# Optimization experiments

Hardware: AMD Instinct MI355X
Metric: run time of the kernel (lower is better)

## Reference

```python
import jax, jax.numpy as jnp
import numpy as np

N, n, D1, D2 = 16, 1024, 64, 64


def setup_inputs() -> dict:
    key = jax.random.key(0)
    ks = jax.random.split(key, 17)
    f = lambda k, shape: jax.random.normal(k, shape, dtype=jnp.float32)
    return {
        "A": f(ks[0], (N, n, n)),
        "X": f(ks[1], (N, n, D1)),
        "coeffs": f(ks[2], (5,)),
        "wA1": f(ks[3], (1, D1)),
        "wA2": f(ks[4], (1, D1)),
        "w11": f(ks[5], (D2, D1)),
        "w12": f(ks[6], (D2, D1)),
        "w13": f(ks[7], (D2, 1)),
        "w14": f(ks[8], (D2, 1)),
        "w15": f(ks[9], (D2, 1)),
        "w16": f(ks[10], (D2, 1)),
        "w21": f(ks[11], (D2, D1)),
        "w22": f(ks[12], (D2, D1)),
        "w23": f(ks[13], (D2, 1)),
        "w24": f(ks[14], (D2, 1)),
        "w25": f(ks[15], (D2, 1)),
        "w26": f(ks[16], (D2, 1)),
    }


def reference(A, X, coeffs, wA1, wA2, w11, w12, w13, w14, w15, w16,
              w21, w22, w23, w24, w25, w26):
    nn_ = A.shape[-1]
    diag = jnp.diagonal(A, axis1=-2, axis2=-1)          # (N, n)
    mean_diag = diag.mean(-1)                            # (N,)
    rowmean = A.mean(-1)                                 # (N, n) mean over columns
    mean_all = rowmean.mean(-1)                          # (N,)
    mean_X = X.mean(1)                                   # (N, D1)

    p1 = X @ wA1[0]                                      # (N, n)   Linear(D1->1) per node
    p2 = mean_X @ wA2[0]                                 # (N,)     Linear(D1->1) on mean

    # adjacency transform: scalar-weighted A + scalar stats + symmetrized row stats
    A_t = (coeffs[0] * A
           + (coeffs[1] * mean_all + coeffs[2] * mean_diag + p2)[:, None, None]
           + coeffs[3] * (rowmean[:, None, :] + rowmean[:, :, None])
           + coeffs[4] * (diag[:, None, :] + diag[:, :, None])
           + p1[:, None, :] + p1[:, :, None])             # (N, n, n)

    def node_transform(w_x, w_mx, w_col, w_diag, w_mdiag, w_mall):
        per_graph = (mean_X @ w_mx.T                      # (N, D2)
                     + mean_diag[:, None] * w_mdiag[:, 0][None, :]
                     + mean_all[:, None] * w_mall[:, 0][None, :])
        return (jnp.einsum('bnd,ed->bne', X, w_x)         # (N, n, D2)
                + rowmean[:, :, None] * w_col[:, 0]
                + diag[:, :, None] * w_diag[:, 0]
                + per_graph[:, None, :])

    X1_t = node_transform(w11, w12, w13, w14, w15, w16)
    X2_t = node_transform(w21, w22, w23, w24, w25, w26)

    out = A_t @ X2_t / nn_ + X1_t                         # (N, n, D2)
    return (A_t, out)
```

## Files before the change

### kernel.cpp

```cpp
#include <hip/hip_runtime.h>
#include <hip/hip_bf16.h>

#define NGRAPH 16
#define NNODE 1024
#define DDIM 64

typedef __attribute__((ext_vector_type(8))) short bf16x8;
typedef __attribute__((ext_vector_type(4))) float f32x4;

#define OFF_ROWSUM 0
#define OFF_DIAG   16384
#define OFF_P1     32768
#define OFF_R      49152
#define OFF_CS     65536
#define OFF_S      73728
#define OFF_S2P    75840
#define OFF_R2P    92224
#define OFF_BASE0  110656
#define OFF_X2T    1159232

__device__ __forceinline__ unsigned short f2bf(float f) {
    unsigned int u = __float_as_uint(f);
    u = (u + 0x7fffu + ((u >> 16) & 1u)) >> 16;
    return (unsigned short)u;
}

__device__ __forceinline__ float wave_reduce(float v) {
    #pragma unroll
    for (int off = 32; off; off >>= 1) v += __shfl_down(v, off, 64);
    return v;
}

__global__ __launch_bounds__(256) void kA_stats(const float* __restrict__ A,
                                                const float* __restrict__ X,
                                                const float* __restrict__ wA1,
                                                float* __restrict__ rowsum,
                                                float* __restrict__ diagv,
                                                float* __restrict__ p1,
                                                float* __restrict__ colsum_part) {
    if (blockIdx.x < NGRAPH * NNODE / 4) {
        int row  = blockIdx.x * 4 + (threadIdx.x >> 6);
        int lane = threadIdx.x & 63;
        const float4* b4 = (const float4*)(A + (size_t)row * NNODE);
        float sum = 0.f;
        #pragma unroll
        for (int it = 0; it < 4; ++it) {
            float4 v = b4[lane + it * 64];
            sum += v.x + v.y + v.z + v.w;
        }
        sum = wave_reduce(sum);
        if (lane == 0) {
            rowsum[row] = sum;
            int i = row & (NNODE - 1);
            diagv[row] = ((const float*)b4)[i];
        }
    } else {
        int bid  = blockIdx.x - NGRAPH * NNODE / 4;
        int b    = bid >> 3;
        int blk  = bid & 7;
        int wv   = threadIdx.x >> 6;
        int lane = threadIdx.x & 63;
        float w = wA1[lane];
        float cs = 0.f;
        int row0 = blk * 128 + wv * 32;
        const float* Xb = X + (size_t)b * NNODE * DDIM;
        for (int rI = 0; rI < 32; ++rI) {
            int i = row0 + rI;
            float x = Xb[i * DDIM + lane];
            cs += x;
            float v = wave_reduce(x * w);
            if (lane == 0) p1[b * NNODE + i] = v;
        }
        __shared__ float csl[4][64];
        csl[wv][lane] = cs;
        __syncthreads();
        if (threadIdx.x < 64) {
            float t = csl[0][lane] + csl[1][lane] + csl[2][lane] + csl[3][lane];
            colsum_part[(b * 8 + blk) * 64 + lane] = t;
        }
    }
}

__global__ __launch_bounds__(256) void kB_nodes(const float* __restrict__ X,
                                                const float* __restrict__ coeffs,
                                                const float* __restrict__ wA2,
                                                const float* __restrict__ w11,
                                                const float* __restrict__ w12,
                                                const float* __restrict__ w13,
                                                const float* __restrict__ w14,
                                                const float* __restrict__ w15,
                                                const float* __restrict__ w16,
                                                const float* __restrict__ w21,
                                                const float* __restrict__ w22,
                                                const float* __restrict__ w23,
                                                const float* __restrict__ w24,
                                                const float* __restrict__ w25,
                                                const float* __restrict__ w26,
                                                const float* __restrict__ rowsum,
                                                const float* __restrict__ diagv,
                                                const float* __restrict__ colsum_part,
                                                const float* __restrict__ p1g,
                                                float* __restrict__ rws,
                                                float* __restrict__ base0,
                                                unsigned short* __restrict__ x2tg,
                                                float* __restrict__ S2part,
                                                float* __restrict__ R2part,
                                                float* __restrict__ sArr) {
    __shared__ float Xl[64][68];
    __shared__ float w1l[64][68];
    __shared__ float w2l[64][68];
    __shared__ unsigned short X2Tl[64][68];
    __shared__ float rm_l[64], dg_l[64], r_l[64];
    __shared__ float redS[4][64], redR[4][64];
    __shared__ float redA[4], redD[4];
    __shared__ float mxs[64], p2s;
    __shared__ float pg1_l[64], pg2_l[64];

    int b    = blockIdx.x >> 4;
    int tile = blockIdx.x & 15;
    int i0   = tile * 64;
    int tid  = threadIdx.x;
    int e    = tid & 63;
    int wv   = tid >> 6;

    const float* Xg = X + (size_t)b * (NNODE * DDIM) + (size_t)i0 * DDIM;
    #pragma unroll
    for (int it = 0; it < 4; ++it) {
        int g   = it * 256 + tid;
        int row = g >> 4;
        int c4  = (g & 15) << 2;
        float4 v  = ((const float4*)Xg)[g];
        *(float4*)&Xl[row][c4] = v;
        float4 v1 = ((const float4*)w11)[g];
        *(float4*)&w1l[row][c4] = v1;
        float4 v2 = ((const float4*)w21)[g];
        *(float4*)&w2l[row][c4] = v2;
    }

    float sa = 0.f, sd = 0.f;
    for (int i = tid; i < NNODE; i += 256) {
        sa += rowsum[b * NNODE + i];
        sd += diagv[b * NNODE + i];
    }
    sa = wave_reduce(sa); sd = wave_reduce(sd);
    if (e == 0) { redA[wv] = sa; redD[wv] = sd; }
    if (tid < 64) {
        float mx = 0.f;
        for (int k = 0; k < 8; ++k) mx += colsum_part[(b * 8 + k) * 64 + tid];
        mxs[tid] = mx * (1.f / (float)NNODE);
    }
    __syncthreads();
    float mean_all  = (redA[0] + redA[1] + redA[2] + redA[3]) * (1.f / ((float)NNODE * (float)NNODE));
    float mean_diag = (redD[0] + redD[1] + redD[2] + redD[3]) * (1.f / (float)NNODE);
    if (tid < 64) {
        float v = wave_reduce(mxs[tid] * wA2[tid]);
        if (tid == 0) p2s = v;
    }
    if (tid < 64) {
        float a1 = 0.f, a2 = 0.f;
        for (int d = 0; d < 64; ++d) {
            float m = mxs[d];
            a1 += m * w12[tid * 64 + d];
            a2 += m * w22[tid * 64 + d];
        }
        pg1_l[tid] = a1 + mean_diag * w15[tid] + mean_all * w16[tid];
        pg2_l[tid] = a2 + mean_diag * w25[tid] + mean_all * w26[tid];
    }
    float c3 = coeffs[3], c4c = coeffs[4];
    if (tid < 64) {
        float rs  = rowsum[b * NNODE + i0 + tid];
        float dgv = diagv[b * NNODE + i0 + tid];
        float rmv = rs * (1.f / (float)NNODE);
        rm_l[tid] = rmv;
        dg_l[tid] = dgv;
        float rv = c3 * rmv + c4c * dgv + p1g[b * NNODE + i0 + tid];
        r_l[tid] = rv;
        rws[b * NNODE + i0 + tid] = rv;
    }
    __syncthreads();
    if (tile == 0 && tid == 0)
        sArr[b] = coeffs[1] * mean_all + coeffs[2] * mean_diag + p2s;

    float w13e = w13[e], w14e = w14[e], w23e = w23[e], w24e = w24[e];
    float pg1e = pg1_l[e], pg2e = pg2_l[e];

    float acc1[16], acc2[16];
    #pragma unroll
    for (int t = 0; t < 16; ++t) { acc1[t] = 0.f; acc2[t] = 0.f; }

    for (int d0 = 0; d0 < 64; d0 += 4) {
        float4 w1v = *(const float4*)&w1l[e][d0];
        float4 w2v = *(const float4*)&w2l[e][d0];
        #pragma unroll
        for (int t = 0; t < 16; ++t) {
            int li = wv + 4 * t;
            float4 xv = *(const float4*)&Xl[li][d0];
            acc1[t] += xv.x * w1v.x + xv.y * w1v.y + xv.z * w1v.z + xv.w * w1v.w;
            acc2[t] += xv.x * w2v.x + xv.y * w2v.y + xv.z * w2v.z + xv.w * w2v.w;
        }
    }

    float s2acc = 0.f, r2acc = 0.f;
    #pragma unroll
    for (int t = 0; t < 16; ++t) {
        int li = wv + 4 * t;
        int i  = i0 + li;
        float rmv = rm_l[li], dgv = dg_l[li];
        float x2t = acc2[t] + rmv * w23e + dgv * w24e + pg2e;
        float b0  = acc1[t] + rmv * w13e + dgv * w14e + pg1e;
        base0[((size_t)(b * NNODE + i)) * 64 + e] = b0;
        X2Tl[e][li] = f2bf(x2t);
        s2acc += x2t;
        r2acc += r_l[li] * x2t;
    }
    redS[wv][e] = s2acc;
    redR[wv][e] = r2acc;
    __syncthreads();

    for (int k = 0; k < 16; ++k) {
        int ep = wv * 16 + k;
        unsigned short v = X2Tl[ep][e];
        x2tg[((size_t)(b * 64 + ep)) * NNODE + i0 + e] = v;
    }
    if (tid < 64) {
        float s2 = redS[0][tid] + redS[1][tid] + redS[2][tid] + redS[3][tid];
        float r2 = redR[0][tid] + redR[1][tid] + redR[2][tid] + redR[3][tid];
        S2part[(b * 16 + tile) * 64 + tid] = s2;
        R2part[(b * 16 + tile) * 64 + tid] = r2;
    }
}

__global__ __launch_bounds__(256) void kC_main(const float* __restrict__ A,
                                               const float* __restrict__ coeffs,
                                               const float* __restrict__ sArr,
                                               const float* __restrict__ rArr,
                                               const unsigned short* __restrict__ x2tg,
                                               const float* __restrict__ base0,
                                               const float* __restrict__ S2part,
                                               const float* __restrict__ R2part,
                                               float* __restrict__ At,
                                               float* __restrict__ outp) {
    __shared__ unsigned short Al[2][16][132];
    __shared__ float r_lds[1024];
    __shared__ float s2_lds[64], r2_lds[64];

    int b    = blockIdx.x >> 6;
    int tile = blockIdx.x & 63;
    int i0   = tile * 16;
    int tid  = threadIdx.x;

    float4 rv = ((const float4*)(rArr + b * NNODE))[tid];
    *(float4*)&r_lds[tid * 4] = rv;
    if (tid < 64) {
        float s2 = 0.f, r2 = 0.f;
        #pragma unroll
        for (int t = 0; t < 16; ++t) {
            s2 += S2part[(b * 16 + t) * 64 + tid];
            r2 += R2part[(b * 16 + t) * 64 + tid];
        }
        s2_lds[tid] = s2 * (1.f / (float)NNODE);
        r2_lds[tid] = r2 * (1.f / (float)NNODE);
    }

    float sb  = sArr[b];
    float c0  = coeffs[0];
    float c0n = c0 * (1.f / (float)NNODE);

    int arow = tid >> 4;
    int acol = (tid & 15) * 8;
    const float* Ab  = A  + ((size_t)(b * NNODE + i0 + arow)) * NNODE + acol;
    float*       Atb = At + ((size_t)(b * NNODE + i0 + arow)) * NNODE + acol;

    int lane = tid & 63, wv = tid >> 6;
    int m = lane & 15, quad = lane >> 4;
    int e = wv * 16 + m;
    const unsigned short* Bg = x2tg + ((size_t)(b * 64 + e)) * NNODE + quad * 8;

    float4 a0 = *(const float4*)(Ab);
    float4 a1 = *(const float4*)(Ab + 4);

    f32x4 acc = {0.f, 0.f, 0.f, 0.f};

    __syncthreads();

    float bse = sb + r_lds[i0 + arow];

    for (int kt = 0; kt < 8; ++kt) {
        bf16x8 bf0 = *(const bf16x8*)(Bg + kt * 128);
        bf16x8 bf1 = *(const bf16x8*)(Bg + kt * 128 + 32);
        bf16x8 bf2 = *(const bf16x8*)(Bg + kt * 128 + 64);
        bf16x8 bf3 = *(const bf16x8*)(Bg + kt * 128 + 96);

        int cidx = kt * 128 + acol;
        float4 rj0 = *(const float4*)&r_lds[cidx];
        float4 rj1 = *(const float4*)&r_lds[cidx + 4];
        f32x4 t0, t1;
        t0.x = fmaf(c0, a0.x, bse + rj0.x);
        t0.y = fmaf(c0, a0.y, bse + rj0.y);
        t0.z = fmaf(c0, a0.z, bse + rj0.z);
        t0.w = fmaf(c0, a0.w, bse + rj0.w);
        t1.x = fmaf(c0, a1.x, bse + rj1.x);
        t1.y = fmaf(c0, a1.y, bse + rj1.y);
        t1.z = fmaf(c0, a1.z, bse + rj1.z);
        t1.w = fmaf(c0, a1.w, bse + rj1.w);
        *(f32x4*)(Atb + kt * 128)     = t0;
        *(f32x4*)(Atb + kt * 128 + 4) = t1;

        uint4 pk;
        pk.x = (unsigned int)f2bf(a0.x) | ((unsigned int)f2bf(a0.y) << 16);
        pk.y = (unsigned int)f2bf(a0.z) | ((unsigned int)f2bf(a0.w) << 16);
        pk.z = (unsigned int)f2bf(a1.x) | ((unsigned int)f2bf(a1.y) << 16);
        pk.w = (unsigned int)f2bf(a1.z) | ((unsigned int)f2bf(a1.w) << 16);
        *(uint4*)&Al[kt & 1][arow][acol] = pk;

        if (kt < 7) {
            a0 = *(const float4*)(Ab + (kt + 1) * 128);
            a1 = *(const float4*)(Ab + (kt + 1) * 128 + 4);
        }

        asm volatile("s_waitcnt lgkmcnt(0)\n\ts_barrier" ::: "memory");

        bf16x8 av0 = *(const bf16x8*)&Al[kt & 1][m][quad * 8];
        bf16x8 av1 = *(const bf16x8*)&Al[kt & 1][m][32 + quad * 8];
        bf16x8 av2 = *(const bf16x8*)&Al[kt & 1][m][64 + quad * 8];
        bf16x8 av3 = *(const bf16x8*)&Al[kt & 1][m][96 + quad * 8];
        acc = __builtin_amdgcn_mfma_f32_16x16x32_bf16(av0, bf0, acc, 0, 0, 0);
        acc = __builtin_amdgcn_mfma_f32_16x16x32_bf16(av1, bf1, acc, 0, 0, 0);
        acc = __builtin_amdgcn_mfma_f32_16x16x32_bf16(av2, bf2, acc, 0, 0, 0);
        acc = __builtin_amdgcn_mfma_f32_16x16x32_bf16(av3, bf3, acc, 0, 0, 0);
    }

    float s2 = s2_lds[e];
    float r2 = r2_lds[e];
    #pragma unroll
    for (int reg = 0; reg < 4; ++reg) {
        int i = i0 + quad * 4 + reg;
        float v = acc[reg] * c0n
                + base0[((size_t)(b * NNODE + i)) * 64 + e]
                + (sb + r_lds[i]) * s2 + r2;
        outp[((size_t)(b * NNODE + i)) * 64 + e] = v;
    }
}

extern "C" void kernel_launch(void* const* d_in, const int* in_sizes, int n_in,
                              void* d_out, int out_size, void* d_ws, size_t ws_size,
                              hipStream_t stream) {
    const float* A      = (const float*)d_in[0];
    const float* X      = (const float*)d_in[1];
    const float* coeffs = (const float*)d_in[2];
    const float* wA1    = (const float*)d_in[3];
    const float* wA2    = (const float*)d_in[4];
    const float* w11    = (const float*)d_in[5];
    const float* w12    = (const float*)d_in[6];
    const float* w13    = (const float*)d_in[7];
    const float* w14    = (const float*)d_in[8];
    const float* w15    = (const float*)d_in[9];
    const float* w16    = (const float*)d_in[10];
    const float* w21    = (const float*)d_in[11];
    const float* w22    = (const float*)d_in[12];
    const float* w23    = (const float*)d_in[13];
    const float* w24    = (const float*)d_in[14];
    const float* w25    = (const float*)d_in[15];
    const float* w26    = (const float*)d_in[16];

    float* ws  = (float*)d_ws;
    float* At  = (float*)d_out;
    float* out = (float*)d_out + (size_t)NGRAPH * NNODE * NNODE;

    float* rowsum = ws + OFF_ROWSUM;
    float* diagv  = ws + OFF_DIAG;
    float* p1     = ws + OFF_P1;
    float* rws    = ws + OFF_R;
    float* cspart = ws + OFF_CS;
    float* sArr   = ws + OFF_S;
    float* S2part = ws + OFF_S2P;
    float* R2part = ws + OFF_R2P;
    float* base0  = ws + OFF_BASE0;
    unsigned short* x2tg = (unsigned short*)(ws + OFF_X2T);

    kA_stats<<<NGRAPH * NNODE / 4 + NGRAPH * 8, 256, 0, stream>>>(
        A, X, wA1, rowsum, diagv, p1, cspart);
    kB_nodes<<<NGRAPH * 16, 256, 0, stream>>>(
        X, coeffs, wA2, w11, w12, w13, w14, w15, w16,
        w21, w22, w23, w24, w25, w26,
        rowsum, diagv, cspart, p1,
        rws, base0, x2tg, S2part, R2part, sArr);
    kC_main<<<NGRAPH * 64, 256, 0, stream>>>(
        A, coeffs, sArr, rws, x2tg, base0, S2part, R2part, At, out);
}
```

Baseline: 202.3 us.

## Prefetch B fragments, use packed bf16 convert, nontemporal stores, split per-graph work across waves

In the main fused kernel, the bf16 X2^T fragments are now prefetched one k-tile ahead, mirroring the existing A prefetch, and the k loop is fully unrolled. The per-element software bf16 rounding is replaced by the hardware packed convert instruction, and the A_t and output stores plus the base0 read become nontemporal to avoid polluting cache. In the stats/transform kernel, the per-graph reductions that wave 0 did serially are spread across four waves. Together these aim to hide global load latency and trim ALU work, at the cost of more registers and possible rounding differences in NaN/edge cases.

```diff
diff --git a/kernel.cpp b/kernel.cpp
--- a/kernel.cpp
+++ b/kernel.cpp
@@ -23,6 +23,12 @@
     unsigned int u = __float_as_uint(f);
     u = (u + 0x7fffu + ((u >> 16) & 1u)) >> 16;
     return (unsigned short)u;
+}
+
+__device__ __forceinline__ unsigned int cvt_pk_bf16(float lo, float hi) {
+    unsigned int r;
+    asm("v_cvt_pk_bf16_f32 %0, %1, %2" : "=v"(r) : "v"(lo), "v"(hi));
+    return r;
 }
 
 __device__ __forceinline__ float wave_reduce(float v) {
@@ -152,30 +158,28 @@
     __syncthreads();
     float mean_all  = (redA[0] + redA[1] + redA[2] + redA[3]) * (1.f / ((float)NNODE * (float)NNODE));
     float mean_diag = (redD[0] + redD[1] + redD[2] + redD[3]) * (1.f / (float)NNODE);
-    if (tid < 64) {
-        float v = wave_reduce(mxs[tid] * wA2[tid]);
-        if (tid == 0) p2s = v;
-    }
-    if (tid < 64) {
-        float a1 = 0.f, a2 = 0.f;
-        for (int d = 0; d < 64; ++d) {
-            float m = mxs[d];
-            a1 += m * w12[tid * 64 + d];
-            a2 += m * w22[tid * 64 + d];
-        }
-        pg1_l[tid] = a1 + mean_diag * w15[tid] + mean_all * w16[tid];
-        pg2_l[tid] = a2 + mean_diag * w25[tid] + mean_all * w26[tid];
-    }
     float c3 = coeffs[3], c4c = coeffs[4];
-    if (tid < 64) {
-        float rs  = rowsum[b * NNODE + i0 + tid];
-        float dgv = diagv[b * NNODE + i0 + tid];
+
+    if (wv == 0) {
+        float a1 = 0.f;
+        for (int d = 0; d < 64; ++d) a1 += mxs[d] * w12[e * 64 + d];
+        pg1_l[e] = a1 + mean_diag * w15[e] + mean_all * w16[e];
+    } else if (wv == 1) {
+        float a2 = 0.f;
+        for (int d = 0; d < 64; ++d) a2 += mxs[d] * w22[e * 64 + d];
+        pg2_l[e] = a2 + mean_diag * w25[e] + mean_all * w26[e];
+    } else if (wv == 2) {
+        float v = wave_reduce(mxs[e] * wA2[e]);
+        if (e == 0) p2s = v;
+    } else {
+        float rs  = rowsum[b * NNODE + i0 + e];
+        float dgv = diagv[b * NNODE + i0 + e];
         float rmv = rs * (1.f / (float)NNODE);
-        rm_l[tid] = rmv;
-        dg_l[tid] = dgv;
-        float rv = c3 * rmv + c4c * dgv + p1g[b * NNODE + i0 + tid];
-        r_l[tid] = rv;
-        rws[b * NNODE + i0 + tid] = rv;
+        rm_l[e] = rmv;
+        dg_l[e] = dgv;
+        float rv = c3 * rmv + c4c * dgv + p1g[b * NNODE + i0 + e];
+        r_l[e] = rv;
+        rws[b * NNODE + i0 + e] = rv;
     }
     __syncthreads();
     if (tile == 0 && tid == 0)
@@ -278,6 +282,10 @@
 
     float4 a0 = *(const float4*)(Ab);
     float4 a1 = *(const float4*)(Ab + 4);
+    bf16x8 bf0 = *(const bf16x8*)(Bg);
+    bf16x8 bf1 = *(const bf16x8*)(Bg + 32);
+    bf16x8 bf2 = *(const bf16x8*)(Bg + 64);
+    bf16x8 bf3 = *(const bf16x8*)(Bg + 96);
 
     f32x4 acc = {0.f, 0.f, 0.f, 0.f};
 
@@ -285,12 +293,8 @@
 
     float bse = sb + r_lds[i0 + arow];
 
+    #pragma unroll
     for (int kt = 0; kt < 8; ++kt) {
-        bf16x8 bf0 = *(const bf16x8*)(Bg + kt * 128);
-        bf16x8 bf1 = *(const bf16x8*)(Bg + kt * 128 + 32);
-        bf16x8 bf2 = *(const bf16x8*)(Bg + kt * 128 + 64);
-        bf16x8 bf3 = *(const bf16x8*)(Bg + kt * 128 + 96);
-
         int cidx = kt * 128 + acol;
         float4 rj0 = *(const float4*)&r_lds[cidx];
         float4 rj1 = *(const float4*)&r_lds[cidx + 4];
@@ -303,19 +307,24 @@
         t1.y = fmaf(c0, a1.y, bse + rj1.y);
         t1.z = fmaf(c0, a1.z, bse + rj1.z);
         t1.w = fmaf(c0, a1.w, bse + rj1.w);
-        *(f32x4*)(Atb + kt * 128)     = t0;
-        *(f32x4*)(Atb + kt * 128 + 4) = t1;
+        __builtin_nontemporal_store(t0, (f32x4*)(Atb + kt * 128));
+        __builtin_nontemporal_store(t1, (f32x4*)(Atb + kt * 128 + 4));
 
         uint4 pk;
-        pk.x = (unsigned int)f2bf(a0.x) | ((unsigned int)f2bf(a0.y) << 16);
-        pk.y = (unsigned int)f2bf(a0.z) | ((unsigned int)f2bf(a0.w) << 16);
-        pk.z = (unsigned int)f2bf(a1.x) | ((unsigned int)f2bf(a1.y) << 16);
-        pk.w = (unsigned int)f2bf(a1.z) | ((unsigned int)f2bf(a1.w) << 16);
+        pk.x = cvt_pk_bf16(a0.x, a0.y);
+        pk.y = cvt_pk_bf16(a0.z, a0.w);
+        pk.z = cvt_pk_bf16(a1.x, a1.y);
+        pk.w = cvt_pk_bf16(a1.z, a1.w);
         *(uint4*)&Al[kt & 1][arow][acol] = pk;
 
+        bf16x8 n0, n1, n2, n3;
         if (kt < 7) {
             a0 = *(const float4*)(Ab + (kt + 1) * 128);
             a1 = *(const float4*)(Ab + (kt + 1) * 128 + 4);
+            n0 = *(const bf16x8*)(Bg + (kt + 1) * 128);
+            n1 = *(const bf16x8*)(Bg + (kt + 1) * 128 + 32);
+            n2 = *(const bf16x8*)(Bg + (kt + 1) * 128 + 64);
+            n3 = *(const bf16x8*)(Bg + (kt + 1) * 128 + 96);
         }
 
         asm volatile("s_waitcnt lgkmcnt(0)\n\ts_barrier" ::: "memory");
@@ -328,6 +337,8 @@
         acc = __builtin_amdgcn_mfma_f32_16x16x32_bf16(av1, bf1, acc, 0, 0, 0);
         acc = __builtin_amdgcn_mfma_f32_16x16x32_bf16(av2, bf2, acc, 0, 0, 0);
         acc = __builtin_amdgcn_mfma_f32_16x16x32_bf16(av3, bf3, acc, 0, 0, 0);
+
+        if (kt < 7) { bf0 = n0; bf1 = n1; bf2 = n2; bf3 = n3; }
     }
 
     float s2 = s2_lds[e];
@@ -335,10 +346,9 @@
     #pragma unroll
     for (int reg = 0; reg < 4; ++reg) {
         int i = i0 + quad * 4 + reg;
-        float v = acc[reg] * c0n
-                + base0[((size_t)(b * NNODE + i)) * 64 + e]
-                + (sb + r_lds[i]) * s2 + r2;
-        outp[((size_t)(b * NNODE + i)) * 64 + e] = v;
+        float bval = __builtin_nontemporal_load(base0 + ((size_t)(b * NNODE + i)) * 64 + e);
+        float v = acc[reg] * c0n + bval + (sb + r_lds[i]) * s2 + r2;
+        __builtin_nontemporal_store(v, outp + ((size_t)(b * NNODE + i)) * 64 + e);
     }
 }
 
```

Measured after the change: 214.9 us. 1.06x slower.
